# Performance work log

Hardware: AMD Instinct MI355X
Metric: run time of the kernel (lower is better)

The kernel has to match this reference:

```python
import jax, jax.numpy as jnp
import numpy as np
import math

B, S, HID = 2, 4096, 2048
H, D, C = 16, 128, 256  # heads, head_dim, chunk (block) size
NC = S // C


def _build_slopes(n):
    # faithful port of MiniMaxText01LinearAttention._build_slope_tensor
    def p2(m):
        start = 2.0 ** (-(2.0 ** (-(math.log2(m) - 3))))
        return [start * (start ** i) for i in range(m)]
    if math.log2(n).is_integer():
        sl = p2(n)
    else:
        cp = 2 ** math.floor(math.log2(n))
        sl = p2(cp) + p2(2 * cp)[0::2][: n - cp]
    return np.asarray(sl, dtype=np.float32).reshape(n, 1, 1)


def setup_inputs() -> dict:
    key = jax.random.key(0)
    k1, k2, k3, k4 = jax.random.split(key, 4)
    x = jax.random.normal(k1, (B, S, HID), dtype=jnp.float32)
    w_qkv = jax.random.normal(k2, (HID, 3 * H * D), dtype=jnp.float32) * 0.02
    w_gate = jax.random.normal(k3, (HID, H * D), dtype=jnp.float32) * 0.02
    w_out = jax.random.normal(k4, (H * D, HID), dtype=jnp.float32) * 0.02
    slopes = jnp.asarray(_build_slopes(H))  # [H,1,1]
    return {"x": x, "w_qkv": w_qkv, "w_gate": w_gate, "w_out": w_out, "slopes": slopes}


def _to_chunks(t):
    # [B,S,H*D] -> [NC,B,H,C,D]
    return (t.reshape(B, S, H, D)
             .transpose(0, 2, 1, 3)          # [B,H,S,D]
             .reshape(B, H, NC, C, D)
             .transpose(2, 0, 1, 3, 4))      # [NC,B,H,C,D]


def _lightning_attn(q, k, v, slopes):
    # q,k,v: [NC,B,H,C,D]; slopes: [H,1,1]
    s = slopes
    pos = jnp.arange(C, dtype=jnp.float32)
    q_decay = jnp.exp(-s * (pos + 1.0).reshape(1, C, 1))        # [H,C,1]
    k_decay = jnp.exp(-s * (C - 1.0 - pos).reshape(1, C, 1))    # [H,C,1]
    idx = pos[:, None] - pos[None, :]                            # [C,C]
    diag_decay = jnp.where(idx >= 0, jnp.exp(-s * idx), 0.0)     # [H,C,C]
    block_decay = jnp.exp(-s * float(C))[None]                   # [1,H,1,1]

    def step(kv, qkv_c):
        qc, kc, vc = qkv_c  # each [B,H,C,D]
        # intra-chunk (causal, decayed)
        scores = jnp.einsum('bhid,bhjd->bhij', qc, kc) * diag_decay
        o = jnp.einsum('bhij,bhjd->bhid', scores, vc)
        # inter-chunk via recurrent state kv: [B,H,D,D]
        o = o + jnp.einsum('bhid,bhde->bhie', qc * q_decay, kv)
        kv = block_decay * kv + jnp.einsum('bhjd,bhje->bhde', kc * k_decay, vc)
        return kv, o

    kv0 = jnp.zeros((B, H, D, D), dtype=q.dtype)
    _, outs = jax.lax.scan(step, kv0, (q, k, v))  # outs: [NC,B,H,C,D]
    return (outs.transpose(1, 2, 0, 3, 4)          # [B,H,NC,C,D]
                .reshape(B, H, S, D)
                .transpose(0, 2, 1, 3)
                .reshape(B, S, H * D))


def reference(x, w_qkv, w_gate, w_out, slopes):
    qkv = jax.nn.silu(x @ w_qkv)                   # act on fused qkv (hidden_act=silu)
    q, k, v = jnp.split(qkv, 3, axis=-1)
    attn = _lightning_attn(_to_chunks(q), _to_chunks(k), _to_chunks(v), slopes)
    gate = jax.nn.sigmoid(x @ w_gate)              # output gate
    return (gate * attn) @ w_out
```

## Files before the change

kernel.cpp:

```cpp
#include <hip/hip_runtime.h>

typedef __bf16 bf16;
typedef __bf16 bf16x8 __attribute__((ext_vector_type(8)));
typedef __bf16 bf16x4 __attribute__((ext_vector_type(4)));
typedef float  f32x4  __attribute__((ext_vector_type(4)));

#define B_   2
#define S_   4096
#define HID_ 2048
#define H_   16
#define D_   128
#define C_   256
#define NC_  16
#define M_   (B_*S_)
#define K_   2048

typedef __attribute__((address_space(1))) const void gas_t;
typedef __attribute__((address_space(3))) void las_t;

__global__ void cvt_kernel(const float* __restrict__ x,
                           const float* __restrict__ wqkv,
                           const float* __restrict__ wgate,
                           const float* __restrict__ wout,
                           bf16* __restrict__ xb, bf16* __restrict__ wT) {
    __shared__ float tile[32][33];
    int bid = blockIdx.x, tid = threadIdx.x;
    if (bid < 8192) {
        int idx = (bid * 256 + tid) * 8;
        float4 f0 = *(const float4*)(x + idx);
        float4 f1 = *(const float4*)(x + idx + 4);
        bf16x8 o;
        o[0] = (bf16)f0.x; o[1] = (bf16)f0.y; o[2] = (bf16)f0.z; o[3] = (bf16)f0.w;
        o[4] = (bf16)f1.x; o[5] = (bf16)f1.y; o[6] = (bf16)f1.z; o[7] = (bf16)f1.w;
        *(bf16x8*)(xb + idx) = o;
        return;
    }
    bid -= 8192;
    int k0 = (bid & 63) * 32, n0 = (bid >> 6) * 32;
    const float* src; int ld, col0;
    if (n0 < 6144)      { src = wqkv;  ld = 6144; col0 = n0; }
    else if (n0 < 8192) { src = wgate; ld = 2048; col0 = n0 - 6144; }
    else                { src = wout;  ld = 2048; col0 = n0 - 8192; }
    int tx = tid & 31, ty = tid >> 5;
#pragma unroll
    for (int i = 0; i < 4; i++) {
        int kk = ty + i * 8;
        tile[kk][tx] = src[(size_t)(k0 + kk) * ld + col0 + tx];
    }
    __syncthreads();
#pragma unroll
    for (int i = 0; i < 4; i++) {
        int nn = ty + i * 8;
        wT[(size_t)(n0 + nn) * K_ + k0 + tx] = (bf16)tile[tx][nn];
    }
}

#define DSRA(dst, buf, tb) do {                                              \
    const bf16* _p = &As[buf][wr][0];                                        \
    _Pragma("unroll")                                                        \
    for (int _t = 0; _t < 4; _t++) {                                         \
        const int _r = ((tb) + _t) * 16 + l15;                               \
        dst[_t][0] = *(const bf16x8*)(_p + _r * 64 + ps0);                   \
        dst[_t][1] = *(const bf16x8*)(_p + _r * 64 + ps1);                   \
    }                                                                        \
} while (0)

#define DSRB(dst, buf, tb) do {                                              \
    const bf16* _p = &Bs[buf][wch][0];                                       \
    _Pragma("unroll")                                                        \
    for (int _t = 0; _t < 2; _t++) {                                         \
        const int _r = bro + ((tb) + _t) * 16 + l15;                         \
        dst[_t][0] = *(const bf16x8*)(_p + _r * 64 + ps0);                   \
        dst[_t][1] = *(const bf16x8*)(_p + _r * 64 + ps1);                   \
    }                                                                        \
} while (0)

#define STAGE_A(buf, h, kt) do {                                             \
    const bf16* _s = Ag + (size_t)(h) * (128 * K_) + (kt) * 64;              \
    bf16* _d = &As[buf][h][srow * 64 + sslot * 8];                           \
    __builtin_amdgcn_global_load_lds((gas_t*)_s, (las_t*)_d, 16, 0, 0);      \
    __builtin_amdgcn_global_load_lds((gas_t*)(_s + (size_t)64 * K_),         \
                                     (las_t*)(_d + 4096), 16, 0, 0);         \
} while (0)

#define STAGE_B(buf, h, kt) do {                                             \
    const bf16* _s = Bg + (size_t)(h) * (128 * K_) + (kt) * 64;              \
    bf16* _d = &Bs[buf][h][srow * 64 + sslot * 8];                           \
    __builtin_amdgcn_global_load_lds((gas_t*)_s, (las_t*)_d, 16, 0, 0);      \
    __builtin_amdgcn_global_load_lds((gas_t*)(_s + (size_t)64 * K_),         \
                                     (las_t*)(_d + 4096), 16, 0, 0);         \
} while (0)

#define MM8(afr, bfr, ib, jb) do {                                           \
    _Pragma("unroll")                                                        \
    for (int _i = 0; _i < 4; _i++)                                           \
        _Pragma("unroll")                                                    \
        for (int _j = 0; _j < 2; _j++)                                       \
            _Pragma("unroll")                                                \
            for (int _k = 0; _k < 2; _k++)                                   \
                acc[(ib) + _i][(jb) + _j] =                                  \
                    __builtin_amdgcn_mfma_f32_16x16x32_bf16(                 \
                        afr[_i][_k], bfr[_j][_k],                            \
                        acc[(ib) + _i][(jb) + _j], 0, 0, 0);                 \
} while (0)

#define PTAIL(...) do {                                                      \
    __builtin_amdgcn_s_barrier();                                            \
    asm volatile("s_waitcnt lgkmcnt(0)" ::: "memory");                       \
    __builtin_amdgcn_s_setprio(1);                                           \
    __VA_ARGS__;                                                             \
    __builtin_amdgcn_s_setprio(0);                                           \
    __builtin_amdgcn_s_barrier();                                            \
} while (0)

#define VMC6 asm volatile("s_waitcnt vmcnt(6)" ::: "memory")
#define VMC0 asm volatile("s_waitcnt vmcnt(0)" ::: "memory")

template <int MODE>
__global__ __launch_bounds__(512, 2) void gemm_kernel(
        const bf16* __restrict__ A, const bf16* __restrict__ Bm,
        bf16* __restrict__ qo, bf16* __restrict__ ko,
        bf16* __restrict__ vo, bf16* __restrict__ go,
        float* __restrict__ out) {
    __shared__ __align__(16) bf16 As[2][2][128 * 64];
    __shared__ __align__(16) bf16 Bs[2][2][128 * 64];
    const int m0 = blockIdx.x * 256, n0 = blockIdx.y * 256;
    const int tid = threadIdx.x, lane = tid & 63, wid = tid >> 6;
    const int quad = lane >> 4, l15 = lane & 15;
    const int wr = wid >> 2, wc = wid & 3;
    const int wch = wc >> 1, bro = (wc & 1) * 64;
    const int srow = tid >> 3, sslot = tid & 7;
    const int lcol = (sslot ^ (srow & 7)) * 8;
    const int ps0 = ((quad)     ^ (l15 & 7)) * 8;
    const int ps1 = ((quad + 4) ^ (l15 & 7)) * 8;
    const bf16* Ag = A  + (size_t)(m0 + srow) * K_ + lcol;
    const bf16* Bg = Bm + (size_t)(n0 + srow) * K_ + lcol;

    f32x4 acc[8][4] = {};
    bf16x8 aLo[4][2], aHi[4][2], bLo[2][2], bHi[2][2];

    STAGE_A(0, 0, 0); STAGE_A(0, 1, 0);
    STAGE_B(0, 0, 0); STAGE_B(0, 1, 0);
    STAGE_B(1, 0, 1); STAGE_B(1, 1, 1);
    STAGE_A(1, 0, 1);
    VMC6;
    __builtin_amdgcn_s_barrier();

#pragma unroll 1
    for (int it = 0; it < 16; ++it) {
        const bool last = (it == 15);
        const int t2 = 2 * it + 2, t3 = 2 * it + 3;
        DSRA(aLo, 0, 0); DSRB(bLo, 0, 0);
        STAGE_A(1, 1, 2 * it + 1);
        PTAIL(MM8(aLo, bLo, 0, 0));
        DSRB(bHi, 0, 2);
        PTAIL(MM8(aLo, bHi, 0, 2));
        DSRA(aHi, 0, 4);
        if (!last) { STAGE_B(0, 0, t2); STAGE_B(0, 1, t2); }
        PTAIL(MM8(aHi, bLo, 4, 0));
        if (!last) STAGE_A(0, 0, t2);
        if (last) VMC0; else VMC6;
        PTAIL(MM8(aHi, bHi, 4, 2));
        DSRA(aLo, 1, 0); DSRB(bLo, 1, 0);
        if (!last) STAGE_A(0, 1, t2);
        PTAIL(MM8(aLo, bLo, 0, 0));
        DSRB(bHi, 1, 2);
        PTAIL(MM8(aLo, bHi, 0, 2));
        DSRA(aHi, 1, 4);
        if (!last) { STAGE_B(1, 0, t3); STAGE_B(1, 1, t3); }
        PTAIL(MM8(aHi, bLo, 4, 0));
        if (!last) STAGE_A(1, 0, t3);
        if (last) VMC0; else VMC6;
        PTAIL(MM8(aHi, bHi, 4, 2));
    }

    const int rb = m0 + wr * 128;
    if (MODE == 0) {
        bf16* outb = (n0 < 2048) ? qo : (n0 < 4096) ? ko : (n0 < 6144) ? vo : go;
        const bool silu = (n0 < 6144);
        const int cb = (n0 & 2047) + wc * 64;
#pragma unroll
        for (int ti = 0; ti < 8; ti++)
#pragma unroll
            for (int tj = 0; tj < 4; tj++)
#pragma unroll
                for (int r = 0; r < 4; r++) {
                    int row = rb + ti * 16 + quad * 4 + r;
                    int col = cb + tj * 16 + l15;
                    float xv = acc[ti][tj][r];
                    float sg = 1.f / (1.f + __expf(-xv));
                    float av = silu ? xv * sg : sg;
                    outb[(size_t)row * 2048 + col] = (bf16)av;
                }
    } else {
        const int cb = n0 + wc * 64;
#pragma unroll
        for (int ti = 0; ti < 8; ti++)
#pragma unroll
            for (int tj = 0; tj < 4; tj++)
#pragma unroll
                for (int r = 0; r < 4; r++) {
                    int row = rb + ti * 16 + quad * 4 + r;
                    int col = cb + tj * 16 + l15;
                    out[(size_t)row * 2048 + col] = acc[ti][tj][r];
                }
    }
}

#undef DSRA
#undef DSRB
#undef STAGE_A
#undef STAGE_B
#undef MM8
#undef PTAIL
#undef VMC6
#undef VMC0

__global__ void transpose_kernel(const bf16* __restrict__ kin,
                                 const bf16* __restrict__ vin,
                                 const float* __restrict__ slopes,
                                 bf16* __restrict__ kT, bf16* __restrict__ vT) {
    __shared__ bf16 tile[64][65];
    int x0 = blockIdx.x * 64, d0 = blockIdx.y * 64;
    int z = blockIdx.z, arr = z >> 5, bh = z & 31, b = bh >> 4, h = bh & 15;
    const bf16* src = arr ? vin : kin;
    bf16* dst = arr ? vT : kT;
    int tx = threadIdx.x, ty = threadIdx.y;
    float fscale = 1.f;
    if (arr == 0)
        fscale = __expf(-slopes[h] * (float)(255 - ((x0 + tx) & 255)));
#pragma unroll
    for (int r = 0; r < 16; r++) {
        int lr = ty * 16 + r;
        tile[lr][tx] = src[(size_t)(b * S_ + x0 + lr) * 2048 + h * 128 + d0 + tx];
    }
    __syncthreads();
#pragma unroll
    for (int r = 0; r < 16; r++) {
        int lr = ty * 16 + r;
        dst[(size_t)(bh * 128 + d0 + lr) * S_ + x0 + tx] =
            (bf16)((float)tile[tx][lr] * fscale);
    }
}

__global__ __launch_bounds__(256) void pass_a_kernel(
        const bf16* __restrict__ kT, const bf16* __restrict__ vT,
        bf16* __restrict__ KVT) {
    int c = blockIdx.x, bh = blockIdx.y;
    int tid = threadIdx.x, lane = tid & 63, wid = tid >> 6;
    int quad = lane >> 4, l15 = lane & 15;
    int e0 = (wid >> 1) * 64, d0 = (wid & 1) * 64;
    const bf16* vb = vT + (size_t)bh * 128 * S_ + c * 256;
    const bf16* kb = kT + (size_t)bh * 128 * S_ + c * 256;
    f32x4 acc[4][4] = {};
    for (int kbs = 0; kbs < 256; kbs += 32) {
        int j0 = kbs + quad * 8;
        bf16x8 af[4], bfr[4];
#pragma unroll
        for (int t = 0; t < 4; t++)
            af[t] = *(const bf16x8*)(vb + (size_t)(e0 + t * 16 + l15) * S_ + j0);
#pragma unroll
        for (int t = 0; t < 4; t++)
            bfr[t] = *(const bf16x8*)(kb + (size_t)(d0 + t * 16 + l15) * S_ + j0);
#pragma unroll
        for (int ti = 0; ti < 4; ti++)
#pragma unroll
            for (int tj = 0; tj < 4; tj++)
                acc[ti][tj] = __builtin_amdgcn_mfma_f32_16x16x32_bf16(
                    af[ti], bfr[tj], acc[ti][tj], 0, 0, 0);
    }
    size_t base = ((size_t)c * 32 + bh) * 16384;
#pragma unroll
    for (int ti = 0; ti < 4; ti++)
#pragma unroll
        for (int tj = 0; tj < 4; tj++)
#pragma unroll
            for (int r = 0; r < 4; r++) {
                int e = e0 + ti * 16 + quad * 4 + r, d = d0 + tj * 16 + l15;
                KVT[base + (size_t)e * 128 + d] = (bf16)acc[ti][tj][r];
            }
}

__global__ void scan_kernel(const bf16* __restrict__ KVT,
                            const float* __restrict__ slopes,
                            bf16* __restrict__ stT) {
    int slice = blockIdx.x, bh = blockIdx.y;
    float s = slopes[bh & 15];
    float bd = __expf(-s * 256.f);
    size_t off = (size_t)slice * 1024 + threadIdx.x * 4;
    float kv0 = 0.f, kv1 = 0.f, kv2 = 0.f, kv3 = 0.f;
    for (int c = 0; c < 16; c++) {
        size_t idx = ((size_t)c * 32 + bh) * 16384 + off;
        bf16x4 st;
        st[0] = (bf16)kv0; st[1] = (bf16)kv1; st[2] = (bf16)kv2; st[3] = (bf16)kv3;
        *(bf16x4*)(stT + idx) = st;
        bf16x4 kvc = *(const bf16x4*)(KVT + idx);
        kv0 = bd * kv0 + (float)kvc[0];
        kv1 = bd * kv1 + (float)kvc[1];
        kv2 = bd * kv2 + (float)kvc[2];
        kv3 = bd * kv3 + (float)kvc[3];
    }
}

__global__ __launch_bounds__(256) void pass_c_kernel(
        const bf16* __restrict__ q, const bf16* __restrict__ kk,
        const bf16* __restrict__ vT, const bf16* __restrict__ stT,
        const bf16* __restrict__ gate, const float* __restrict__ slopes,
        bf16* __restrict__ og) {
    __shared__ __align__(16) bf16 P[256 * 72];
    __shared__ float dtab[257];
    int c = blockIdx.x, bh = blockIdx.y, b = bh >> 4, h = bh & 15;
    int tid = threadIdx.x, lane = tid & 63, wid = tid >> 6;
    int quad = lane >> 4, l15 = lane & 15;
    int i0 = wid * 64;
    float s = slopes[h];
    dtab[tid] = __expf(-s * (float)tid);
    if (tid == 0) dtab[256] = __expf(-s * 256.f);
    __syncthreads();
    const bf16* qb = q  + ((size_t)(b * S_ + c * 256)) * 2048 + h * 128;
    const bf16* kb = kk + ((size_t)(b * S_ + c * 256)) * 2048 + h * 128;
    const bf16* vb = vT + (size_t)bh * 128 * S_ + c * 256;
    const bf16* st = stT + ((size_t)c * 32 + bh) * 16384;
    f32x4 acc[4][8] = {};

    for (int kbs = 0; kbs < 128; kbs += 32) {
        bf16x8 af[4];
#pragma unroll
        for (int t = 0; t < 4; t++)
            af[t] = *(const bf16x8*)(qb + (size_t)(i0 + t * 16 + l15) * 2048 + kbs + quad * 8);
#pragma unroll
        for (int te = 0; te < 8; te++) {
            bf16x8 bfr = *(const bf16x8*)(st + (size_t)(te * 16 + l15) * 128 + kbs + quad * 8);
#pragma unroll
            for (int t = 0; t < 4; t++)
                acc[t][te] = __builtin_amdgcn_mfma_f32_16x16x32_bf16(
                    af[t], bfr, acc[t][te], 0, 0, 0);
        }
    }
#pragma unroll
    for (int t = 0; t < 4; t++) {
        float qd[4];
#pragma unroll
        for (int r = 0; r < 4; r++) qd[r] = dtab[i0 + t * 16 + quad * 4 + r + 1];
#pragma unroll
        for (int te = 0; te < 8; te++)
#pragma unroll
            for (int r = 0; r < 4; r++) acc[t][te][r] *= qd[r];
    }

    for (int jt = 0; jt <= wid; jt++) {
        f32x4 sacc[4][4] = {};
        for (int kbs = 0; kbs < 128; kbs += 32) {
            bf16x8 af[4], bkr[4];
#pragma unroll
            for (int t = 0; t < 4; t++)
                af[t] = *(const bf16x8*)(qb + (size_t)(i0 + t * 16 + l15) * 2048 + kbs + quad * 8);
#pragma unroll
            for (int t = 0; t < 4; t++)
                bkr[t] = *(const bf16x8*)(kb + (size_t)(jt * 64 + t * 16 + l15) * 2048 + kbs + quad * 8);
#pragma unroll
            for (int ti = 0; ti < 4; ti++)
#pragma unroll
                for (int tj = 0; tj < 4; tj++)
                    sacc[ti][tj] = __builtin_amdgcn_mfma_f32_16x16x32_bf16(
                        af[ti], bkr[tj], sacc[ti][tj], 0, 0, 0);
        }
#pragma unroll
        for (int ti = 0; ti < 4; ti++)
#pragma unroll
            for (int tj = 0; tj < 4; tj++)
#pragma unroll
                for (int r = 0; r < 4; r++) {
                    int i = i0 + ti * 16 + quad * 4 + r;
                    int j = jt * 64 + tj * 16 + l15;
                    int diff = i - j;
                    float pv = (diff >= 0) ? sacc[ti][tj][r] * dtab[diff] : 0.f;
                    P[i * 72 + tj * 16 + l15] = (bf16)pv;
                }
#pragma unroll
        for (int k2 = 0; k2 < 64; k2 += 32) {
            bf16x8 af[4];
#pragma unroll
            for (int t = 0; t < 4; t++)
                af[t] = *(const bf16x8*)&P[(i0 + t * 16 + l15) * 72 + k2 + quad * 8];
#pragma unroll
            for (int te = 0; te < 8; te++) {
                bf16x8 bfr = *(const bf16x8*)(vb + (size_t)(te * 16 + l15) * S_ + jt * 64 + k2 + quad * 8);
#pragma unroll
                for (int t = 0; t < 4; t++)
                    acc[t][te] = __builtin_amdgcn_mfma_f32_16x16x32_bf16(
                        af[t], bfr, acc[t][te], 0, 0, 0);
            }
        }
    }

    const bf16* gb = gate + ((size_t)(b * S_ + c * 256)) * 2048 + h * 128;
    bf16* ob = og + ((size_t)(b * S_ + c * 256)) * 2048 + h * 128;
#pragma unroll
    for (int ti = 0; ti < 4; ti++)
#pragma unroll
        for (int te = 0; te < 8; te++)
#pragma unroll
            for (int r = 0; r < 4; r++) {
                int i = i0 + ti * 16 + quad * 4 + r;
                int e = te * 16 + l15;
                float gv = (float)gb[(size_t)i * 2048 + e];
                ob[(size_t)i * 2048 + e] = (bf16)(acc[ti][te][r] * gv);
            }
}

extern "C" void kernel_launch(void* const* d_in, const int* in_sizes, int n_in,
                              void* d_out, int out_size, void* d_ws, size_t ws_size,
                              hipStream_t stream) {
    const float* x      = (const float*)d_in[0];
    const float* wqkv   = (const float*)d_in[1];
    const float* wgate  = (const float*)d_in[2];
    const float* wout   = (const float*)d_in[3];
    const float* slopes = (const float*)d_in[4];
    float* out = (float*)d_out;

    bf16* wT   = (bf16*)d_ws;
    bf16* xb   = wT   + (size_t)10240 * 2048;
    bf16* qb   = xb   + (size_t)8192 * 2048;
    bf16* kbuf = qb   + (size_t)8192 * 2048;
    bf16* vbuf = kbuf + (size_t)8192 * 2048;
    bf16* gbuf = vbuf + (size_t)8192 * 2048;
    bf16* kT   = xb;
    bf16* vT   = (bf16*)d_out;
    bf16* KVT  = vT + (size_t)32 * 128 * 4096;
    bf16* stT  = KVT + (size_t)16 * 32 * 16384;

    cvt_kernel<<<dim3(28672), dim3(256), 0, stream>>>(x, wqkv, wgate, wout, xb, wT);
    gemm_kernel<0><<<dim3(32, 32), dim3(512), 0, stream>>>(
        xb, wT, qb, kbuf, vbuf, gbuf, (float*)nullptr);
    transpose_kernel<<<dim3(64, 2, 64), dim3(64, 4), 0, stream>>>(
        kbuf, vbuf, slopes, kT, vT);
    pass_a_kernel<<<dim3(16, 32), dim3(256), 0, stream>>>(kT, vT, KVT);
    scan_kernel<<<dim3(16, 32), dim3(256), 0, stream>>>(KVT, slopes, stT);
    pass_c_kernel<<<dim3(16, 32), dim3(256), 0, stream>>>(
        qb, kbuf, vT, stT, gbuf, slopes, vbuf);
    gemm_kernel<1><<<dim3(32, 8), dim3(512), 0, stream>>>(
        vbuf, wT + (size_t)8192 * 2048, nullptr, nullptr, nullptr, nullptr, out);
}
```

Before: 640.1 us.

## Fuse K/V transpose and decay scaling into QKV GEMM epilogue

Removes the standalone transpose kernel. The QKV GEMM epilogue now stages the SiLU-activated K and V tiles in shared memory with an XOR swizzle, then writes them transposed (K also scaled by its per-position decay) straight into the kT/vT layouts. V is no longer written row-major, which saves one full write and one re-read of K and V. The cost is extra epilogue work, a block-wide sync in the GEMM, and reuse of the LDS buffer for staging.

```diff
diff --git a/kernel.cpp b/kernel.cpp
--- a/kernel.cpp
+++ b/kernel.cpp
@@ -56,7 +56,7 @@
 }
 
 #define DSRA(dst, buf, tb) do {                                              \
-    const bf16* _p = &As[buf][wr][0];                                        \
+    const bf16* _p = SMEM + ((buf) * 2 + wr) * 8192;                         \
     _Pragma("unroll")                                                        \
     for (int _t = 0; _t < 4; _t++) {                                         \
         const int _r = ((tb) + _t) * 16 + l15;                               \
@@ -66,7 +66,7 @@
 } while (0)
 
 #define DSRB(dst, buf, tb) do {                                              \
-    const bf16* _p = &Bs[buf][wch][0];                                       \
+    const bf16* _p = SMEM + 32768 + ((buf) * 2 + wch) * 8192;                \
     _Pragma("unroll")                                                        \
     for (int _t = 0; _t < 2; _t++) {                                         \
         const int _r = bro + ((tb) + _t) * 16 + l15;                         \
@@ -77,7 +77,7 @@
 
 #define STAGE_A(buf, h, kt) do {                                             \
     const bf16* _s = Ag + (size_t)(h) * (128 * K_) + (kt) * 64;              \
-    bf16* _d = &As[buf][h][srow * 64 + sslot * 8];                           \
+    bf16* _d = SMEM + ((buf) * 2 + (h)) * 8192 + srow * 64 + sslot * 8;      \
     __builtin_amdgcn_global_load_lds((gas_t*)_s, (las_t*)_d, 16, 0, 0);      \
     __builtin_amdgcn_global_load_lds((gas_t*)(_s + (size_t)64 * K_),         \
                                      (las_t*)(_d + 4096), 16, 0, 0);         \
@@ -85,7 +85,7 @@
 
 #define STAGE_B(buf, h, kt) do {                                             \
     const bf16* _s = Bg + (size_t)(h) * (128 * K_) + (kt) * 64;              \
-    bf16* _d = &Bs[buf][h][srow * 64 + sslot * 8];                           \
+    bf16* _d = SMEM + 32768 + ((buf) * 2 + (h)) * 8192 + srow * 64 + sslot * 8; \
     __builtin_amdgcn_global_load_lds((gas_t*)_s, (las_t*)_d, 16, 0, 0);      \
     __builtin_amdgcn_global_load_lds((gas_t*)(_s + (size_t)64 * K_),         \
                                      (las_t*)(_d + 4096), 16, 0, 0);         \
@@ -120,10 +120,10 @@
 __global__ __launch_bounds__(512, 2) void gemm_kernel(
         const bf16* __restrict__ A, const bf16* __restrict__ Bm,
         bf16* __restrict__ qo, bf16* __restrict__ ko,
-        bf16* __restrict__ vo, bf16* __restrict__ go,
+        bf16* __restrict__ go, bf16* __restrict__ vTd,
+        bf16* __restrict__ kTd, const float* __restrict__ slopes,
         float* __restrict__ out) {
-    __shared__ __align__(16) bf16 As[2][2][128 * 64];
-    __shared__ __align__(16) bf16 Bs[2][2][128 * 64];
+    __shared__ __align__(16) bf16 SMEM[65536];
     const int m0 = blockIdx.x * 256, n0 = blockIdx.y * 256;
     const int tid = threadIdx.x, lane = tid & 63, wid = tid >> 6;
     const int quad = lane >> 4, l15 = lane & 15;
@@ -176,9 +176,67 @@
 
     const int rb = m0 + wr * 128;
     if (MODE == 0) {
-        bf16* outb = (n0 < 2048) ? qo : (n0 < 4096) ? ko : (n0 < 6144) ? vo : go;
-        const bool silu = (n0 < 6144);
-        const int cb = (n0 & 2047) + wc * 64;
+        const int kind = n0 >> 11;
+        const int cb = n0 & 2047;
+        if (kind != 2) {
+            bf16* outb = (kind == 0) ? qo : (kind == 1) ? ko : go;
+            const bool silu = (kind < 3);
+#pragma unroll
+            for (int ti = 0; ti < 8; ti++)
+#pragma unroll
+                for (int tj = 0; tj < 4; tj++)
+#pragma unroll
+                    for (int r = 0; r < 4; r++) {
+                        int row = rb + ti * 16 + quad * 4 + r;
+                        int col = cb + wc * 64 + tj * 16 + l15;
+                        float xv = acc[ti][tj][r];
+                        float sg = 1.f / (1.f + __expf(-xv));
+                        float av = silu ? xv * sg : sg;
+                        outb[(size_t)row * 2048 + col] = (bf16)av;
+                    }
+        }
+        if (kind == 1 || kind == 2) {
+#pragma unroll
+            for (int ti = 0; ti < 8; ti++)
+#pragma unroll
+                for (int tj = 0; tj < 4; tj++) {
+                    int c = wc * 64 + tj * 16 + l15;
+                    int s0 = wr * 128 + ti * 16 + quad * 4;
+                    bf16x4 t4;
+#pragma unroll
+                    for (int r = 0; r < 4; r++) {
+                        float xv = acc[ti][tj][r];
+                        float sg = 1.f / (1.f + __expf(-xv));
+                        t4[r] = (bf16)(xv * sg);
+                    }
+                    int byt = (c * 512 + s0 * 2) ^ ((c & 7) << 4);
+                    *(bf16x4*)((char*)SMEM + byt) = t4;
+                }
+            __syncthreads();
+            bf16* dstT = (kind == 2) ? vTd : kTd;
+            const int bq = m0 >> 12, sbase = m0 & 4095, hb = cb >> 7;
+            const int l = tid & 31, rg = tid >> 5;
+#pragma unroll 1
+            for (int p = 0; p < 16; ++p) {
+                int c = p * 16 + rg;
+                int byt = (c * 512 + l * 16) ^ ((c & 7) << 4);
+                bf16x8 vv = *(const bf16x8*)((const char*)SMEM + byt);
+                int h = hb + (c >> 7), d = c & 127;
+                if (kind == 1) {
+                    float sl = slopes[h];
+                    float e = __expf(-sl * (float)(255 - l * 8));
+                    float rr = __expf(sl);
+#pragma unroll
+                    for (int i = 0; i < 8; i++) {
+                        vv[i] = (bf16)((float)vv[i] * e);
+                        e *= rr;
+                    }
+                }
+                *(bf16x8*)(dstT + ((size_t)(bq * 16 + h) * 128 + d) * (size_t)S_
+                           + sbase + l * 8) = vv;
+            }
+        }
+    } else {
 #pragma unroll
         for (int ti = 0; ti < 8; ti++)
 #pragma unroll
@@ -186,22 +244,7 @@
 #pragma unroll
                 for (int r = 0; r < 4; r++) {
                     int row = rb + ti * 16 + quad * 4 + r;
-                    int col = cb + tj * 16 + l15;
-                    float xv = acc[ti][tj][r];
-                    float sg = 1.f / (1.f + __expf(-xv));
-                    float av = silu ? xv * sg : sg;
-                    outb[(size_t)row * 2048 + col] = (bf16)av;
-                }
-    } else {
-        const int cb = n0 + wc * 64;
-#pragma unroll
-        for (int ti = 0; ti < 8; ti++)
-#pragma unroll
-            for (int tj = 0; tj < 4; tj++)
-#pragma unroll
-                for (int r = 0; r < 4; r++) {
-                    int row = rb + ti * 16 + quad * 4 + r;
-                    int col = cb + tj * 16 + l15;
+                    int col = n0 + wc * 64 + tj * 16 + l15;
                     out[(size_t)row * 2048 + col] = acc[ti][tj][r];
                 }
     }
@@ -215,33 +258,6 @@
 #undef PTAIL
 #undef VMC6
 #undef VMC0
-
-__global__ void transpose_kernel(const bf16* __restrict__ kin,
-                                 const bf16* __restrict__ vin,
-                                 const float* __restrict__ slopes,
-                                 bf16* __restrict__ kT, bf16* __restrict__ vT) {
-    __shared__ bf16 tile[64][65];
-    int x0 = blockIdx.x * 64, d0 = blockIdx.y * 64;
-    int z = blockIdx.z, arr = z >> 5, bh = z & 31, b = bh >> 4, h = bh & 15;
-    const bf16* src = arr ? vin : kin;
-    bf16* dst = arr ? vT : kT;
-    int tx = threadIdx.x, ty = threadIdx.y;
-    float fscale = 1.f;
-    if (arr == 0)
-        fscale = __expf(-slopes[h] * (float)(255 - ((x0 + tx) & 255)));
-#pragma unroll
-    for (int r = 0; r < 16; r++) {
-        int lr = ty * 16 + r;
-        tile[lr][tx] = src[(size_t)(b * S_ + x0 + lr) * 2048 + h * 128 + d0 + tx];
-    }
-    __syncthreads();
-#pragma unroll
-    for (int r = 0; r < 16; r++) {
-        int lr = ty * 16 + r;
-        dst[(size_t)(bh * 128 + d0 + lr) * S_ + x0 + tx] =
-            (bf16)((float)tile[tx][lr] * fscale);
-    }
-}
 
 __global__ __launch_bounds__(256) void pass_a_kernel(
         const bf16* __restrict__ kT, const bf16* __restrict__ vT,
@@ -423,22 +439,21 @@
     bf16* xb   = wT   + (size_t)10240 * 2048;
     bf16* qb   = xb   + (size_t)8192 * 2048;
     bf16* kbuf = qb   + (size_t)8192 * 2048;
-    bf16* vbuf = kbuf + (size_t)8192 * 2048;
-    bf16* gbuf = vbuf + (size_t)8192 * 2048;
-    bf16* kT   = xb;
+    bf16* kTn  = kbuf + (size_t)8192 * 2048;
+    bf16* gbuf = kTn  + (size_t)8192 * 2048;
+    bf16* ogb  = kTn;
     bf16* vT   = (bf16*)d_out;
     bf16* KVT  = vT + (size_t)32 * 128 * 4096;
     bf16* stT  = KVT + (size_t)16 * 32 * 16384;
 
     cvt_kernel<<<dim3(28672), dim3(256), 0, stream>>>(x, wqkv, wgate, wout, xb, wT);
     gemm_kernel<0><<<dim3(32, 32), dim3(512), 0, stream>>>(
-        xb, wT, qb, kbuf, vbuf, gbuf, (float*)nullptr);
-    transpose_kernel<<<dim3(64, 2, 64), dim3(64, 4), 0, stream>>>(
-        kbuf, vbuf, slopes, kT, vT);
-    pass_a_kernel<<<dim3(16, 32), dim3(256), 0, stream>>>(kT, vT, KVT);
+        xb, wT, qb, kbuf, gbuf, vT, kTn, slopes, (float*)nullptr);
+    pass_a_kernel<<<dim3(16, 32), dim3(256), 0, stream>>>(kTn, vT, KVT);
     scan_kernel<<<dim3(16, 32), dim3(256), 0, stream>>>(KVT, slopes, stT);
     pass_c_kernel<<<dim3(16, 32), dim3(256), 0, stream>>>(
-        qb, kbuf, vT, stT, gbuf, slopes, vbuf);
+        qb, kbuf, vT, stT, gbuf, slopes, ogb);
     gemm_kernel<1><<<dim3(32, 8), dim3(512), 0, stream>>>(
-        vbuf, wT + (size_t)8192 * 2048, nullptr, nullptr, nullptr, nullptr, out);
-}
+        ogb, wT + (size_t)8192 * 2048, nullptr, nullptr, nullptr, nullptr,
+        nullptr, nullptr, out);
+}
```

Result: faster. 606.8 us (-5.2%).
